# Performance work log

Hardware: AMD Instinct MI355X
Metric: run time of the kernel (lower is better)

Reference implementation:

```python
import jax, jax.numpy as jnp
import numpy as np

B, S, D_MODEL, FFN, P = 8, 4096, 256, 1024, 8
BLK = 256  # token block size for the max-plus reduction


def setup_inputs() -> dict:
    key = jax.random.key(0)
    ks = jax.random.split(key, 12)
    x = jax.random.normal(ks[0], (B, S, D_MODEL), jnp.float32)
    # TropicalLinear params (additive semiring weights -> small scale)
    Wt = 0.05 * jax.random.normal(ks[1], (FFN, D_MODEL), jnp.float32)
    bt = 0.05 * jax.random.normal(ks[2], (FFN,), jnp.float32)
    # LFDualActivation: per-channel piecewise-linear convex (max) and concave (min)
    # branches, blended by a per-channel sigmoid gate alpha ('blend' mode).
    sl_cvx = 1.0 + 0.1 * jax.random.normal(ks[3], (FFN, P), jnp.float32)
    of_cvx = 0.1 * jax.random.normal(ks[4], (FFN, P), jnp.float32)
    sl_ccv = 1.0 + 0.1 * jax.random.normal(ks[5], (FFN, P), jnp.float32)
    of_ccv = 0.1 * jax.random.normal(ks[6], (FFN, P), jnp.float32)
    alpha = jnp.zeros((FFN,), jnp.float32)
    # Classical branch
    Wc = jax.random.normal(ks[7], (D_MODEL, FFN), jnp.float32) / np.sqrt(D_MODEL)
    bc = jnp.zeros((FFN,), jnp.float32)
    # Gate: init per source (weight ~0, bias +2.0 -> g ~ 0.88 tropical)
    Wg = 0.01 * jax.random.normal(ks[8], (D_MODEL, FFN), jnp.float32)
    bg = 2.0 * jnp.ones((FFN,), jnp.float32)
    # Down projection
    Wd = jax.random.normal(ks[9], (FFN, D_MODEL), jnp.float32) / np.sqrt(FFN)
    bd = jnp.zeros((D_MODEL,), jnp.float32)
    return {"x": x, "Wt": Wt, "bt": bt, "sl_cvx": sl_cvx, "of_cvx": of_cvx,
            "sl_ccv": sl_ccv, "of_ccv": of_ccv, "alpha": alpha,
            "Wc": Wc, "bc": bc, "Wg": Wg, "bg": bg, "Wd": Wd, "bd": bd}


def reference(x, Wt, bt, sl_cvx, of_cvx, sl_ccv, of_ccv, alpha, Wc, bc, Wg, bg, Wd, bd):
    Bx, Sx, D = x.shape
    T = Bx * Sx
    xf = x.reshape(T, D)
    xb = xf.reshape(T // BLK, BLK, D)
    s = jax.nn.sigmoid(alpha)  # [FFN]

    def blk_fn(xx):  # xx: [BLK, D]
        # Tropical (max-plus) linear: t[n,m] = max_k(xx[n,k] + Wt[m,k]) + bt[m]
        t = jnp.max(xx[:, None, :] + Wt[None, :, :], axis=-1) + bt  # [BLK, FFN]
        # LF dual activation: blend of convex (max of lines) and concave (min of lines)
        z = t[:, :, None]  # [BLK, FFN, 1]
        cvx = jnp.max(z * sl_cvx[None] + of_cvx[None], axis=-1)
        ccv = jnp.min(z * sl_ccv[None] + of_ccv[None], axis=-1)
        return s * cvx + (1.0 - s) * ccv  # [BLK, FFN]

    trop = jax.lax.map(blk_fn, xb).reshape(T, FFN)  # dropout = identity (eval)
    classical = jax.nn.gelu(xf @ Wc + bc, approximate=False)
    g = jax.nn.sigmoid(xf @ Wg + bg)
    fused = g * trop + (1.0 - g) * classical
    out = fused @ Wd + bd  # final dropout = identity (eval)
    return out.reshape(Bx, Sx, D)
```

## Files before the change

### kernel.cpp

```cpp
#include <hip/hip_runtime.h>

#define TTOK 32768
#define DM   256
#define NF   1024
#define KMAX 32

typedef __attribute__((ext_vector_type(8))) unsigned short ushort8;
typedef __attribute__((ext_vector_type(8))) __bf16 bf16x8;
typedef __attribute__((ext_vector_type(4))) float floatx4;

constexpr size_t O_SLOT = 0;
constexpr size_t O_S    = 256;
constexpr size_t O_WCT  = O_S    + 4096;
constexpr size_t O_WGT  = O_WCT  + (size_t)NF*DM*2;
constexpr size_t O_WDT  = O_WGT  + (size_t)NF*DM*2;
constexpr size_t O_WTT  = O_WDT  + (size_t)DM*NF*2;
constexpr size_t O_XBF  = O_WTT  + (size_t)DM*NF*4;
constexpr size_t O_CNT  = O_XBF  + (size_t)TTOK*DM*2;
constexpr size_t O_CIDX = O_CNT  + (size_t)TTOK*4;
constexpr size_t O_CVAL = O_CIDX + (size_t)TTOK*KMAX*4;
constexpr size_t O_FUSD = O_CVAL + (size_t)TTOK*KMAX*4;

__device__ __forceinline__ float bf2f(unsigned short u) {
    union { unsigned int i; float f; } c; c.i = ((unsigned int)u) << 16; return c.f;
}
__device__ __forceinline__ unsigned short f2bf(float v) {
    union { float f; unsigned int i; } c; c.f = v;
    unsigned int b = c.i;
    return (unsigned short)((b + 0x7FFFu + ((b >> 16) & 1u)) >> 16);
}
__device__ __forceinline__ float sigm(float z) { return 1.0f / (1.0f + __expf(-z)); }
__device__ __forceinline__ float gelu_f(float x) {
    return x * sigm(1.59576912f * (x + 0.044715f * x * x * x));
}
__device__ __forceinline__ void g2lds16(const unsigned short* g, unsigned short* l) {
    __builtin_amdgcn_global_load_lds((const __attribute__((address_space(1))) unsigned int*)g,
                                     (__attribute__((address_space(3))) unsigned int*)l, 16, 0, 0);
}

__global__ void pack_kernel(const float* __restrict__ Wt, const float* __restrict__ alpha,
                            const float* __restrict__ Wc, const float* __restrict__ Wg,
                            const float* __restrict__ Wd,
                            unsigned short* __restrict__ Wct, unsigned short* __restrict__ Wgt,
                            unsigned short* __restrict__ WdT, float* __restrict__ WtT,
                            float* __restrict__ s, unsigned int* __restrict__ slot) {
    int e = blockIdx.x * 256 + threadIdx.x;
    if (e == 0) *slot = 0u;
    { int f = e >> 8, k = e & 255;
      Wct[e] = f2bf(Wc[k * NF + f]);
      Wgt[e] = f2bf(Wg[k * NF + f]); }
    { int n = e >> 10, k = e & 1023;
      WdT[e] = f2bf(Wd[k * DM + n]); }
    { int d = e >> 10, f = e & 1023;
      WtT[e] = Wt[f * DM + d]; }
    if (e < NF) s[e] = sigm(alpha[e]);
}

__global__ void minmax_kernel(const float* __restrict__ Wt, unsigned int* __restrict__ slot) {
    int g = blockIdx.x * 256 + threadIdx.x;
    float lm = 0.0f;
    for (int i = g; i < NF * DM; i += 128 * 256) lm = fmaxf(lm, fabsf(Wt[i]));
    #pragma unroll
    for (int o = 32; o > 0; o >>= 1) lm = fmaxf(lm, __shfl_xor(lm, o));
    if ((threadIdx.x & 63) == 0) atomicMax(slot, __float_as_uint(lm));
}

__global__ void cand_kernel(const float* __restrict__ x, const unsigned int* __restrict__ slot,
                            unsigned short* __restrict__ xbf, int* __restrict__ counts,
                            int* __restrict__ cidx, float* __restrict__ cval) {
    int i = blockIdx.x, t = threadIdx.x;
    float v = x[i * DM + t];
    xbf[i * DM + t] = f2bf(v);
    float m = v;
    #pragma unroll
    for (int o = 32; o > 0; o >>= 1) m = fmaxf(m, __shfl_xor(m, o));
    __shared__ float wm[4];
    __shared__ int cnt;
    __shared__ int sidx[KMAX];
    __shared__ float sval[KMAX];
    if ((t & 63) == 0) wm[t >> 6] = m;
    if (t == 0) cnt = 0;
    __syncthreads();
    float xmax = fmaxf(fmaxf(wm[0], wm[1]), fmaxf(wm[2], wm[3]));
    float delta = 2.0f * __uint_as_float(*slot);
    float thr = xmax - delta;
    if (v >= thr) {
        int p = atomicAdd(&cnt, 1);
        if (p < KMAX) { sidx[p] = t * NF; sval[p] = v; }
    }
    __syncthreads();
    int c = cnt;
    if (t == 0) counts[i] = c;
    if (t < (c < KMAX ? c : KMAX)) {
        cidx[i * KMAX + t] = sidx[t];
        cval[i * KMAX + t] = sval[t];
    }
}

#define LDSS 32
#define KPAD 33
__global__ __launch_bounds__(512, 4) void gemm1_kernel(
    const unsigned short* __restrict__ A,
    const unsigned short* __restrict__ Bct,
    const unsigned short* __restrict__ Bgt,
    const float* __restrict__ bc, const float* __restrict__ bg,
    const int* __restrict__ counts, const int* __restrict__ cidx,
    const float* __restrict__ cval, const float* __restrict__ x,
    const float* __restrict__ WtT, const float* __restrict__ bt,
    const float* __restrict__ slx, const float* __restrict__ ofx,
    const float* __restrict__ slc, const float* __restrict__ ofc,
    const float* __restrict__ s, unsigned short* __restrict__ fused) {
    __shared__ __align__(16) unsigned short As[128 * LDSS];
    __shared__ __align__(16) unsigned short Bcs[128 * LDSS];
    __shared__ __align__(16) unsigned short Bgs[128 * LDSS];
    __shared__ __align__(8) int sOV[128 * KPAD * 2];
    __shared__ int sCnt[128];
    const int t = threadIdx.x;
    const int bm = blockIdx.x, bf = blockIdx.y;
    const int wave = t >> 6, lane = t & 63;
    const int wm = wave & 1, wn = wave >> 1;
    const int lr = lane & 15, quad = lane >> 4;
    const int srow = wave * 16 + (lane >> 2), scol = (lane & 3) << 3;
    const unsigned short* gA = A   + (size_t)(bm * 128 + srow) * DM + scol;
    const unsigned short* gC = Bct + (size_t)(bf * 128 + srow) * DM + scol;
    const unsigned short* gG = Bgt + (size_t)(bf * 128 + srow) * DM + scol;
    unsigned short* lA = &As[wave * 16 * LDSS];
    unsigned short* lC = &Bcs[wave * 16 * LDSS];
    unsigned short* lG = &Bgs[wave * 16 * LDSS];

    if (t < 128) sCnt[t] = counts[bm * 128 + t];
    for (int e = t; e < 128 * KMAX; e += 512) {
        int m = e >> 5, k = e & 31;
        int c = counts[bm * 128 + m];
        int off = 0; float val = -1e30f;
        if (k < (c < KMAX ? c : KMAX)) {
            off = cidx[(size_t)(bm * 128 + m) * KMAX + k];
            val = cval[(size_t)(bm * 128 + m) * KMAX + k];
        }
        sOV[(m * KPAD + k) * 2]     = off;
        sOV[(m * KPAD + k) * 2 + 1] = __float_as_int(val);
    }

    floatx4 accc[4][2], accg[4][2];
    #pragma unroll
    for (int i = 0; i < 4; i++)
        #pragma unroll
        for (int j = 0; j < 2; j++) { accc[i][j] = (floatx4)0.0f; accg[i][j] = (floatx4)0.0f; }

    for (int k0 = 0; k0 < DM; k0 += 32) {
        __syncthreads();
        g2lds16(gA + k0, lA);
        g2lds16(gC + k0, lC);
        g2lds16(gG + k0, lG);
        __syncthreads();
        bf16x8 af[4], bcf[2], bgf[2];
        #pragma unroll
        for (int mi = 0; mi < 4; mi++)
            af[mi] = *(const bf16x8*)&As[(wm * 64 + mi * 16 + lr) * LDSS + quad * 8];
        #pragma unroll
        for (int ni = 0; ni < 2; ni++) {
            bcf[ni] = *(const bf16x8*)&Bcs[(wn * 32 + ni * 16 + lr) * LDSS + quad * 8];
            bgf[ni] = *(const bf16x8*)&Bgs[(wn * 32 + ni * 16 + lr) * LDSS + quad * 8];
        }
        #pragma unroll
        for (int mi = 0; mi < 4; mi++)
            #pragma unroll
            for (int ni = 0; ni < 2; ni++) {
                accc[mi][ni] = __builtin_amdgcn_mfma_f32_16x16x32_bf16(af[mi], bcf[ni], accc[mi][ni], 0, 0, 0);
                accg[mi][ni] = __builtin_amdgcn_mfma_f32_16x16x32_bf16(af[mi], bgf[ni], accg[mi][ni], 0, 0, 0);
            }
    }

    #pragma unroll
    for (int mi = 0; mi < 4; mi++) {
        const int mb = wm * 64 + mi * 16 + quad * 4;
        int c0 = sCnt[mb], c1 = sCnt[mb + 1], c2 = sCnt[mb + 2], c3 = sCnt[mb + 3];
        int k0c = c0 < KMAX ? c0 : KMAX, k1c = c1 < KMAX ? c1 : KMAX;
        int k2c = c2 < KMAX ? c2 : KMAX, k3c = c3 < KMAX ? c3 : KMAX;
        int km = max(max(k0c, k1c), max(k2c, k3c));
        #pragma unroll
        for (int ni = 0; ni < 2; ni++) {
            const int f = bf * 128 + wn * 32 + ni * 16 + lr;
            float z0 = -1e30f, z1 = -1e30f, z2 = -1e30f, z3 = -1e30f;
            for (int k = 0; k < km; k++) {
                int2 p0 = *(const int2*)&sOV[((mb + 0) * KPAD + k) * 2];
                int2 p1 = *(const int2*)&sOV[((mb + 1) * KPAD + k) * 2];
                int2 p2 = *(const int2*)&sOV[((mb + 2) * KPAD + k) * 2];
                int2 p3 = *(const int2*)&sOV[((mb + 3) * KPAD + k) * 2];
                float w0 = WtT[p0.x + f];
                float w1 = WtT[p1.x + f];
                float w2 = WtT[p2.x + f];
                float w3 = WtT[p3.x + f];
                z0 = fmaxf(z0, __int_as_float(p0.y) + w0);
                z1 = fmaxf(z1, __int_as_float(p1.y) + w1);
                z2 = fmaxf(z2, __int_as_float(p2.y) + w2);
                z3 = fmaxf(z3, __int_as_float(p3.y) + w3);
            }
            if (c0 > KMAX || c1 > KMAX || c2 > KMAX || c3 > KMAX) {
                float zz[4] = { z0, z1, z2, z3 };
                int cc[4] = { c0, c1, c2, c3 };
                #pragma unroll 1
                for (int r = 0; r < 4; r++) if (cc[r] > KMAX) {
                    const float* xr = x + (size_t)(bm * 128 + mb + r) * DM;
                    float m2 = -1e30f;
                    for (int d = 0; d < DM; d++) m2 = fmaxf(m2, xr[d] + WtT[d * NF + f]);
                    zz[r] = m2;
                }
                z0 = zz[0]; z1 = zz[1]; z2 = zz[2]; z3 = zz[3];
            }
            float4 a0 = *(const float4*)(slx + f * 8), a1 = *(const float4*)(slx + f * 8 + 4);
            float4 b0 = *(const float4*)(ofx + f * 8), b1 = *(const float4*)(ofx + f * 8 + 4);
            float4 cc0 = *(const float4*)(slc + f * 8), cc1 = *(const float4*)(slc + f * 8 + 4);
            float4 d0 = *(const float4*)(ofc + f * 8), d1 = *(const float4*)(ofc + f * 8 + 4);
            float btf = bt[f], sf = s[f];
            float bcv = bc[f], bgv = bg[f];
            float zr[4] = { z0, z1, z2, z3 };
            #pragma unroll
            for (int r = 0; r < 4; r++) {
                float z = zr[r] + btf;
                float cvx = fmaf(z, a0.x, b0.x);
                cvx = fmaxf(cvx, fmaf(z, a0.y, b0.y));
                cvx = fmaxf(cvx, fmaf(z, a0.z, b0.z));
                cvx = fmaxf(cvx, fmaf(z, a0.w, b0.w));
                cvx = fmaxf(cvx, fmaf(z, a1.x, b1.x));
                cvx = fmaxf(cvx, fmaf(z, a1.y, b1.y));
                cvx = fmaxf(cvx, fmaf(z, a1.z, b1.z));
                cvx = fmaxf(cvx, fmaf(z, a1.w, b1.w));
                float ccv = fmaf(z, cc0.x, d0.x);
                ccv = fminf(ccv, fmaf(z, cc0.y, d0.y));
                ccv = fminf(ccv, fmaf(z, cc0.z, d0.z));
                ccv = fminf(ccv, fmaf(z, cc0.w, d0.w));
                ccv = fminf(ccv, fmaf(z, cc1.x, d1.x));
                ccv = fminf(ccv, fmaf(z, cc1.y, d1.y));
                ccv = fminf(ccv, fmaf(z, cc1.z, d1.z));
                ccv = fminf(ccv, fmaf(z, cc1.w, d1.w));
                float tv = sf * cvx + (1.0f - sf) * ccv;
                float cpre = accc[mi][ni][r] + bcv;
                float gpre = accg[mi][ni][r] + bgv;
                float g = sigm(gpre);
                float cla = gelu_f(cpre);
                int m = bm * 128 + mb + r;
                fused[(size_t)m * NF + f] = f2bf(g * tv + (1.0f - g) * cla);
            }
        }
    }
}

__global__ __launch_bounds__(512, 4) void gemm2_kernel(
    const unsigned short* __restrict__ A,
    const unsigned short* __restrict__ Bt,
    const float* __restrict__ bd, float* __restrict__ out) {
    __shared__ __align__(16) unsigned short As[128 * LDSS];
    __shared__ __align__(16) unsigned short Bs[128 * LDSS];
    const int t = threadIdx.x;
    const int bm = blockIdx.x, bn = blockIdx.y;
    const int wave = t >> 6, lane = t & 63;
    const int wm = wave & 1, wn = wave >> 1;
    const int lr = lane & 15, quad = lane >> 4;
    const int srow = wave * 16 + (lane >> 2), scol = (lane & 3) << 3;
    const unsigned short* gA = A  + (size_t)(bm * 128 + srow) * NF + scol;
    const unsigned short* gB = Bt + (size_t)(bn * 128 + srow) * NF + scol;
    unsigned short* lA = &As[wave * 16 * LDSS];
    unsigned short* lB = &Bs[wave * 16 * LDSS];

    floatx4 acc[4][2];
    #pragma unroll
    for (int i = 0; i < 4; i++)
        #pragma unroll
        for (int j = 0; j < 2; j++) acc[i][j] = (floatx4)0.0f;

    for (int k0 = 0; k0 < NF; k0 += 32) {
        __syncthreads();
        g2lds16(gA + k0, lA);
        g2lds16(gB + k0, lB);
        __syncthreads();
        bf16x8 af[4], bf_[2];
        #pragma unroll
        for (int mi = 0; mi < 4; mi++)
            af[mi] = *(const bf16x8*)&As[(wm * 64 + mi * 16 + lr) * LDSS + quad * 8];
        #pragma unroll
        for (int ni = 0; ni < 2; ni++)
            bf_[ni] = *(const bf16x8*)&Bs[(wn * 32 + ni * 16 + lr) * LDSS + quad * 8];
        #pragma unroll
        for (int mi = 0; mi < 4; mi++)
            #pragma unroll
            for (int ni = 0; ni < 2; ni++)
                acc[mi][ni] = __builtin_amdgcn_mfma_f32_16x16x32_bf16(af[mi], bf_[ni], acc[mi][ni], 0, 0, 0);
    }
    #pragma unroll
    for (int mi = 0; mi < 4; mi++)
        #pragma unroll
        for (int ni = 0; ni < 2; ni++) {
            int n = bn * 128 + wn * 32 + ni * 16 + lr;
            float bdv = bd[n];
            #pragma unroll
            for (int r = 0; r < 4; r++) {
                int m = bm * 128 + wm * 64 + mi * 16 + quad * 4 + r;
                out[m * DM + n] = acc[mi][ni][r] + bdv;
            }
        }
}

extern "C" void kernel_launch(void* const* d_in, const int* in_sizes, int n_in,
                              void* d_out, int out_size, void* d_ws, size_t ws_size,
                              hipStream_t stream) {
    const float* x     = (const float*)d_in[0];
    const float* Wt    = (const float*)d_in[1];
    const float* bt    = (const float*)d_in[2];
    const float* slx   = (const float*)d_in[3];
    const float* ofx   = (const float*)d_in[4];
    const float* slc   = (const float*)d_in[5];
    const float* ofc   = (const float*)d_in[6];
    const float* alpha = (const float*)d_in[7];
    const float* Wc    = (const float*)d_in[8];
    const float* bc    = (const float*)d_in[9];
    const float* Wg    = (const float*)d_in[10];
    const float* bg    = (const float*)d_in[11];
    const float* Wd    = (const float*)d_in[12];
    const float* bd    = (const float*)d_in[13];
    float* out = (float*)d_out;
    char* ws = (char*)d_ws;

    unsigned int* slot = (unsigned int*)(ws + O_SLOT);
    float* s           = (float*)(ws + O_S);
    unsigned short* Wct = (unsigned short*)(ws + O_WCT);
    unsigned short* Wgt = (unsigned short*)(ws + O_WGT);
    unsigned short* WdT = (unsigned short*)(ws + O_WDT);
    float* WtT          = (float*)(ws + O_WTT);
    unsigned short* xbf = (unsigned short*)(ws + O_XBF);
    int* counts         = (int*)(ws + O_CNT);
    int* cidx           = (int*)(ws + O_CIDX);
    float* cval         = (float*)(ws + O_CVAL);
    unsigned short* fused = (unsigned short*)(ws + O_FUSD);

    pack_kernel<<<1024, 256, 0, stream>>>(Wt, alpha, Wc, Wg, Wd, Wct, Wgt, WdT, WtT, s, slot);
    minmax_kernel<<<128, 256, 0, stream>>>(Wt, slot);
    cand_kernel<<<TTOK, 256, 0, stream>>>(x, slot, xbf, counts, cidx, cval);
    gemm1_kernel<<<dim3(TTOK / 128, NF / 128), 512, 0, stream>>>(
        xbf, Wct, Wgt, bc, bg, counts, cidx, cval, x, WtT, bt,
        slx, ofx, slc, ofc, s, fused);
    gemm2_kernel<<<dim3(TTOK / 128, DM / 128), 512, 0, stream>>>(fused, WdT, bd, out);
}
```

Measured before the change: 354.7 us.

## Alias LDS, pack candidates, stage fused output stores, widen gemm2 K-tile

gemm1 now reuses the GEMM staging LDS for the candidate table, filled after the MFMA loop. Each candidate is packed into one int: a bf16 value plus a 16-bit index. This shrinks LDS use and the per-candidate loads. The fused output is staged through LDS by row group and written as coalesced 16-byte stores instead of scattered 2-byte stores. The grid axes are swapped so neighbouring blocks share the same A rows, and gemm2 loads a 64-wide K tile per sync. Rounding candidate values to bf16 slightly changes the tropical max, and the extra barriers per mi step add some sync cost.

Result: slower. 384.5 us (+8.4%).

```diff
diff --git a/kernel.cpp b/kernel.cpp
--- a/kernel.cpp
+++ b/kernel.cpp
@@ -86,7 +86,7 @@
     float thr = xmax - delta;
     if (v >= thr) {
         int p = atomicAdd(&cnt, 1);
-        if (p < KMAX) { sidx[p] = t * NF; sval[p] = v; }
+        if (p < KMAX) { sidx[p] = t; sval[p] = v; }
     }
     __syncthreads();
     int c = cnt;
@@ -99,6 +99,7 @@
 
 #define LDSS 32
 #define KPAD 33
+#define OSTR 144
 __global__ __launch_bounds__(512, 4) void gemm1_kernel(
     const unsigned short* __restrict__ A,
     const unsigned short* __restrict__ Bct,
@@ -110,13 +111,15 @@
     const float* __restrict__ slx, const float* __restrict__ ofx,
     const float* __restrict__ slc, const float* __restrict__ ofc,
     const float* __restrict__ s, unsigned short* __restrict__ fused) {
-    __shared__ __align__(16) unsigned short As[128 * LDSS];
-    __shared__ __align__(16) unsigned short Bcs[128 * LDSS];
-    __shared__ __align__(16) unsigned short Bgs[128 * LDSS];
-    __shared__ __align__(8) int sOV[128 * KPAD * 2];
-    __shared__ int sCnt[128];
+    __shared__ __align__(16) char smem[25088 + OSTR * 32 * 2];
+    unsigned short* As  = (unsigned short*)smem;
+    unsigned short* Bcs = As + 4096;
+    unsigned short* Bgs = As + 8192;
+    int* sOV  = (int*)smem;
+    int* sCnt = (int*)(smem + 24576);
+    unsigned short* obuf = (unsigned short*)(smem + 25088);
     const int t = threadIdx.x;
-    const int bm = blockIdx.x, bf = blockIdx.y;
+    const int bf = blockIdx.x, bm = blockIdx.y;
     const int wave = t >> 6, lane = t & 63;
     const int wm = wave & 1, wn = wave >> 1;
     const int lr = lane & 15, quad = lane >> 4;
@@ -129,17 +132,6 @@
     unsigned short* lG = &Bgs[wave * 16 * LDSS];
 
     if (t < 128) sCnt[t] = counts[bm * 128 + t];
-    for (int e = t; e < 128 * KMAX; e += 512) {
-        int m = e >> 5, k = e & 31;
-        int c = counts[bm * 128 + m];
-        int off = 0; float val = -1e30f;
-        if (k < (c < KMAX ? c : KMAX)) {
-            off = cidx[(size_t)(bm * 128 + m) * KMAX + k];
-            val = cval[(size_t)(bm * 128 + m) * KMAX + k];
-        }
-        sOV[(m * KPAD + k) * 2]     = off;
-        sOV[(m * KPAD + k) * 2 + 1] = __float_as_int(val);
-    }
 
     floatx4 accc[4][2], accg[4][2];
     #pragma unroll
@@ -170,6 +162,21 @@
                 accg[mi][ni] = __builtin_amdgcn_mfma_f32_16x16x32_bf16(af[mi], bgf[ni], accg[mi][ni], 0, 0, 0);
             }
     }
+    __syncthreads();
+
+    const int PADV = (int)(((unsigned int)f2bf(-1e30f)) << 16);
+    for (int e = t; e < 128 * KMAX; e += 512) {
+        int m = e >> 5, k = e & 31;
+        int c = sCnt[m];
+        int pk = PADV;
+        if (k < (c < KMAX ? c : KMAX)) {
+            int d  = cidx[(size_t)(bm * 128 + m) * KMAX + k];
+            float v = cval[(size_t)(bm * 128 + m) * KMAX + k];
+            pk = (int)(((unsigned int)f2bf(v)) << 16) | d;
+        }
+        sOV[m * KPAD + k] = pk;
+    }
+    __syncthreads();
 
     #pragma unroll
     for (int mi = 0; mi < 4; mi++) {
@@ -180,21 +187,22 @@
         int km = max(max(k0c, k1c), max(k2c, k3c));
         #pragma unroll
         for (int ni = 0; ni < 2; ni++) {
-            const int f = bf * 128 + wn * 32 + ni * 16 + lr;
+            const int fl = wn * 32 + ni * 16 + lr;
+            const int f = bf * 128 + fl;
             float z0 = -1e30f, z1 = -1e30f, z2 = -1e30f, z3 = -1e30f;
             for (int k = 0; k < km; k++) {
-                int2 p0 = *(const int2*)&sOV[((mb + 0) * KPAD + k) * 2];
-                int2 p1 = *(const int2*)&sOV[((mb + 1) * KPAD + k) * 2];
-                int2 p2 = *(const int2*)&sOV[((mb + 2) * KPAD + k) * 2];
-                int2 p3 = *(const int2*)&sOV[((mb + 3) * KPAD + k) * 2];
-                float w0 = WtT[p0.x + f];
-                float w1 = WtT[p1.x + f];
-                float w2 = WtT[p2.x + f];
-                float w3 = WtT[p3.x + f];
-                z0 = fmaxf(z0, __int_as_float(p0.y) + w0);
-                z1 = fmaxf(z1, __int_as_float(p1.y) + w1);
-                z2 = fmaxf(z2, __int_as_float(p2.y) + w2);
-                z3 = fmaxf(z3, __int_as_float(p3.y) + w3);
+                int p0 = sOV[(mb + 0) * KPAD + k];
+                int p1 = sOV[(mb + 1) * KPAD + k];
+                int p2 = sOV[(mb + 2) * KPAD + k];
+                int p3 = sOV[(mb + 3) * KPAD + k];
+                float w0 = WtT[((p0 & 0xFFFF) << 10) + f];
+                float w1 = WtT[((p1 & 0xFFFF) << 10) + f];
+                float w2 = WtT[((p2 & 0xFFFF) << 10) + f];
+                float w3 = WtT[((p3 & 0xFFFF) << 10) + f];
+                z0 = fmaxf(z0, __int_as_float(p0 & 0xFFFF0000) + w0);
+                z1 = fmaxf(z1, __int_as_float(p1 & 0xFFFF0000) + w1);
+                z2 = fmaxf(z2, __int_as_float(p2 & 0xFFFF0000) + w2);
+                z3 = fmaxf(z3, __int_as_float(p3 & 0xFFFF0000) + w3);
             }
             if (c0 > KMAX || c1 > KMAX || c2 > KMAX || c3 > KMAX) {
                 float zz[4] = { z0, z1, z2, z3 };
@@ -239,29 +247,37 @@
                 float gpre = accg[mi][ni][r] + bgv;
                 float g = sigm(gpre);
                 float cla = gelu_f(cpre);
-                int m = bm * 128 + mb + r;
-                fused[(size_t)m * NF + f] = f2bf(g * tv + (1.0f - g) * cla);
-            }
-        }
-    }
-}
-
+                obuf[(wm * 16 + quad * 4 + r) * OSTR + fl] = f2bf(g * tv + (1.0f - g) * cla);
+            }
+        }
+        __syncthreads();
+        {
+            int row = t >> 4, col8 = (t & 15) << 3;
+            int gm = bm * 128 + (row >> 4) * 64 + mi * 16 + (row & 15);
+            ushort8 v = *(const ushort8*)&obuf[row * OSTR + col8];
+            *(ushort8*)&fused[(size_t)gm * NF + bf * 128 + col8] = v;
+        }
+        __syncthreads();
+    }
+}
+
+#define LDS2 64
 __global__ __launch_bounds__(512, 4) void gemm2_kernel(
     const unsigned short* __restrict__ A,
     const unsigned short* __restrict__ Bt,
     const float* __restrict__ bd, float* __restrict__ out) {
-    __shared__ __align__(16) unsigned short As[128 * LDSS];
-    __shared__ __align__(16) unsigned short Bs[128 * LDSS];
+    __shared__ __align__(16) unsigned short As[128 * LDS2];
+    __shared__ __align__(16) unsigned short Bs[128 * LDS2];
     const int t = threadIdx.x;
-    const int bm = blockIdx.x, bn = blockIdx.y;
+    const int bn = blockIdx.x, bm = blockIdx.y;
     const int wave = t >> 6, lane = t & 63;
     const int wm = wave & 1, wn = wave >> 1;
     const int lr = lane & 15, quad = lane >> 4;
-    const int srow = wave * 16 + (lane >> 2), scol = (lane & 3) << 3;
+    const int srow = wave * 8 + (lane >> 3), scol = (lane & 7) << 3;
     const unsigned short* gA = A  + (size_t)(bm * 128 + srow) * NF + scol;
     const unsigned short* gB = Bt + (size_t)(bn * 128 + srow) * NF + scol;
-    unsigned short* lA = &As[wave * 16 * LDSS];
-    unsigned short* lB = &Bs[wave * 16 * LDSS];
+    unsigned short* lA = &As[wave * 8 * LDS2];
+    unsigned short* lB = &Bs[wave * 8 * LDS2];
 
     floatx4 acc[4][2];
     #pragma unroll
@@ -269,23 +285,28 @@
         #pragma unroll
         for (int j = 0; j < 2; j++) acc[i][j] = (floatx4)0.0f;
 
-    for (int k0 = 0; k0 < NF; k0 += 32) {
+    for (int k0 = 0; k0 < NF; k0 += 64) {
         __syncthreads();
         g2lds16(gA + k0, lA);
+        g2lds16(gA + k0 + (size_t)64 * NF, lA + 64 * LDS2);
         g2lds16(gB + k0, lB);
-        __syncthreads();
-        bf16x8 af[4], bf_[2];
-        #pragma unroll
-        for (int mi = 0; mi < 4; mi++)
-            af[mi] = *(const bf16x8*)&As[(wm * 64 + mi * 16 + lr) * LDSS + quad * 8];
-        #pragma unroll
-        for (int ni = 0; ni < 2; ni++)
-            bf_[ni] = *(const bf16x8*)&Bs[(wn * 32 + ni * 16 + lr) * LDSS + quad * 8];
-        #pragma unroll
-        for (int mi = 0; mi < 4; mi++)
+        g2lds16(gB + k0 + (size_t)64 * NF, lB + 64 * LDS2);
+        __syncthreads();
+        #pragma unroll
+        for (int ks = 0; ks < 2; ks++) {
+            bf16x8 af[4], bf_[2];
+            #pragma unroll
+            for (int mi = 0; mi < 4; mi++)
+                af[mi] = *(const bf16x8*)&As[(wm * 64 + mi * 16 + lr) * LDS2 + ks * 32 + quad * 8];
             #pragma unroll
             for (int ni = 0; ni < 2; ni++)
-                acc[mi][ni] = __builtin_amdgcn_mfma_f32_16x16x32_bf16(af[mi], bf_[ni], acc[mi][ni], 0, 0, 0);
+                bf_[ni] = *(const bf16x8*)&Bs[(wn * 32 + ni * 16 + lr) * LDS2 + ks * 32 + quad * 8];
+            #pragma unroll
+            for (int mi = 0; mi < 4; mi++)
+                #pragma unroll
+                for (int ni = 0; ni < 2; ni++)
+                    acc[mi][ni] = __builtin_amdgcn_mfma_f32_16x16x32_bf16(af[mi], bf_[ni], acc[mi][ni], 0, 0, 0);
+        }
     }
     #pragma unroll
     for (int mi = 0; mi < 4; mi++)
@@ -336,8 +357,8 @@
     pack_kernel<<<1024, 256, 0, stream>>>(Wt, alpha, Wc, Wg, Wd, Wct, Wgt, WdT, WtT, s, slot);
     minmax_kernel<<<128, 256, 0, stream>>>(Wt, slot);
     cand_kernel<<<TTOK, 256, 0, stream>>>(x, slot, xbf, counts, cidx, cval);
-    gemm1_kernel<<<dim3(TTOK / 128, NF / 128), 512, 0, stream>>>(
+    gemm1_kernel<<<dim3(NF / 128, TTOK / 128), 512, 0, stream>>>(
         xbf, Wct, Wgt, bc, bg, counts, cidx, cval, x, WtT, bt,
         slx, ofx, slc, ofc, s, fused);
-    gemm2_kernel<<<dim3(TTOK / 128, DM / 128), 512, 0, stream>>>(fused, WdT, bd, out);
-}
+    gemm2_kernel<<<dim3(DM / 128, TTOK / 128), 512, 0, stream>>>(fused, WdT, bd, out);
+}
```
